# Kernel optimization log

Hardware: AMD Instinct MI355X
Metric: run time of the kernel (lower is better)

## Reference

```python
import jax, jax.numpy as jnp
import numpy as np


def _haar_dwt2(x):
    # x: [b, H, W] -> (ll, lh, hl, hh), each [b, H/2, W/2]; orthonormal 2D Haar
    a = x[:, ::2, ::2]
    b = x[:, ::2, 1::2]
    c = x[:, 1::2, ::2]
    d = x[:, 1::2, 1::2]
    ll = (a + b + c + d) * 0.5
    lh = (a + b - c - d) * 0.5  # detail along rows (frames)
    hl = (a - b + c - d) * 0.5  # detail along cols (features)
    hh = (a - b - c + d) * 0.5
    return ll, lh, hl, hh


def _haar_idwt2(ll, lh, hl, hh):
    a = (ll + lh + hl + hh) * 0.5
    b = (ll + lh - hl - hh) * 0.5
    c = (ll - lh + hl - hh) * 0.5
    d = (ll - lh - hl + hh) * 0.5
    B, H2, W2 = ll.shape
    out = jnp.zeros((B, 2 * H2, 2 * W2), ll.dtype)
    out = out.at[:, ::2, ::2].set(a)
    out = out.at[:, ::2, 1::2].set(b)
    out = out.at[:, 1::2, ::2].set(c)
    out = out.at[:, 1::2, 1::2].set(d)
    return out


def _interp_linear_last(x, m):
    # linear interpolation along last dim from linspace(0,1,n) to linspace(0,1,m)
    n = x.shape[-1]
    pos = jnp.linspace(0.0, 1.0, m, dtype=x.dtype) * (n - 1)
    i0 = jnp.clip(jnp.floor(pos).astype(jnp.int32), 0, n - 2)
    w = pos - i0.astype(x.dtype)
    return x[..., i0] * (1.0 - w) + x[..., i0 + 1] * w


def setup_inputs() -> dict:
    key = jax.random.key(0)
    k0, k1, k2 = jax.random.split(key, 3)
    b, f, c, hidden = 128, 256, 512, 2048
    x = jax.random.normal(k0, (b, f, c), dtype=jnp.float32)
    fc1_w = jax.random.normal(k1, (hidden, c), dtype=jnp.float32) * 0.02
    fc1_b = jnp.zeros((hidden,), dtype=jnp.float32)
    fc2_w = jax.random.normal(k2, (c // 2, hidden), dtype=jnp.float32) * 0.02
    fc2_b = jnp.zeros((c // 2,), dtype=jnp.float32)
    return {"x": x, "fc1_w": fc1_w, "fc1_b": fc1_b, "fc2_w": fc2_w, "fc2_b": fc2_b}


def reference(x, fc1_w, fc1_b, fc2_w, fc2_b):
    b, f, c = x.shape
    ll, lh, hl, hh = _haar_dwt2(x)               # [b, f/2, c/2] each
    ll_up = _interp_linear_last(ll, c)           # [b, f/2, c]
    h = jax.nn.gelu(jnp.einsum('bfc,hc->bfh', ll_up, fc1_w) + fc1_b, approximate=False)
    ll_new = jnp.einsum('bfh,oh->bfo', h, fc2_w) + fc2_b  # [b, f/2, c/2]
    return _haar_idwt2(ll_new, lh, hl, hh)       # [b, f, c]
```

## Files before the change

### kernel.cpp

```cpp
#include <hip/hip_runtime.h>
#include <hip/hip_bf16.h>
#include <stdint.h>

typedef __bf16 bf16;
typedef __attribute__((ext_vector_type(8)))  __bf16 bf16x8;
typedef __attribute__((ext_vector_type(16))) float  f32x16;

#define B_DIM 128
#define F_DIM 256
#define C_DIM 512
#define HID   2048
#define C2    256
#define MROWS 16384

static constexpr size_t OFF_W1 = 0;
static constexpr size_t OFF_W2 = 1u << 20;

__device__ __forceinline__ unsigned short bfbits(float f) {
    bf16 h = (bf16)f;
    return __builtin_bit_cast(unsigned short, h);
}
#define SCHED0() __builtin_amdgcn_sched_barrier(0)

__global__ __launch_bounds__(256) void prep_kernel(
    const float* __restrict__ w1, const float* __restrict__ w2,
    bf16* __restrict__ w1pp, bf16* __restrict__ w2pp)
{
    const int blk = blockIdx.x;
    const int t = threadIdx.x;
    if (blk < 2048) {
        int idx = blk * 256 + t;
        int h = idx >> 8, k = idx & 255;
        const float* wrow = w1 + (size_t)h * C_DIM;
        float acc = 0.f;
        int jlo = (k == 0) ? 0 : (int)((float)(k - 1) * (511.0f / 255.0f));
        int jhi = (int)((float)(k + 1) * (511.0f / 255.0f)) + 1;
        if (jhi > 511) jhi = 511;
        for (int j = jlo; j <= jhi; ++j) {
            float pos = (float)j * (255.0f / 511.0f);
            int i0 = (int)pos;
            if (i0 > 254) i0 = 254;
            float w = pos - (float)i0;
            float coef = (i0 == k) ? (1.0f - w) : ((i0 + 1 == k) ? w : 0.0f);
            acc += coef * wrow[j];
        }
        size_t frag = (size_t)(h >> 5) * 16 + (k >> 4);
        size_t lane = (size_t)(((k >> 3) & 1) << 5 | (h & 31));
        w1pp[frag * 512 + lane * 8 + (k & 7)] = (bf16)acc;
    } else {
        int idx2 = (blk - 2048) * 256 + t;
        int c2 = idx2 >> 11, hid = idx2 & 2047;
        float v = w2[(size_t)c2 * HID + hid];
        size_t frag = (size_t)(c2 >> 5) * 128 + (hid >> 4);
        size_t lane = (size_t)(((hid >> 3) & 1) << 5 | (c2 & 31));
        w2pp[frag * 512 + lane * 8 + (hid & 7)] = (bf16)v;
    }
}

__global__ __launch_bounds__(512, 2) void fused_mlp(
    const bf16* __restrict__ w1pp, const bf16* __restrict__ w2pp,
    const float* __restrict__ b1, const float* __restrict__ b2,
    const float* __restrict__ x, float* __restrict__ out)
{
    __shared__ __align__(16) char smem[49152];
    char* hsm = smem + 16384;

    const int tid = threadIdx.x;
    const int l   = tid & 63;
    const int wv  = tid >> 6;
    const int sub = wv >> 2;
    const int sl4 = wv & 3;
    const int R0  = blockIdx.x * 32;
    const char* w1B = (const char*)w1pp;
    const char* w2B = (const char*)w2pp;

    {
        const int r = tid & 31;
        const int s = tid >> 5;
        const int gbf = R0 + r;
        const float* xr0 = x + ((size_t)(gbf >> 7) * F_DIM + (size_t)(gbf & 127) * 2) * C_DIM;
        const float* xr1 = xr0 + C_DIM;
#pragma unroll
        for (int jj = 0; jj < 2; ++jj) {
            int j = s * 2 + jj;
            float4 a[4], b[4];
#pragma unroll
            for (int i = 0; i < 4; ++i) {
                a[i] = ((const float4*)xr0)[j * 4 + i];
                b[i] = ((const float4*)xr1)[j * 4 + i];
            }
            const float* pa = (const float*)a;
            const float* pb = (const float*)b;
            bf16x8 pk;
#pragma unroll
            for (int e = 0; e < 8; ++e)
                pk[e] = (bf16)(0.5f * (pa[2*e] + pa[2*e+1] + pb[2*e] + pb[2*e+1]));
            *(bf16x8*)(smem + s * 1024 + (size_t)((jj << 5) | r) * 16) = pk;
        }
    }
    __syncthreads();

    bf16x8 llr[16];
#pragma unroll
    for (int kf = 0; kf < 16; ++kf)
        llr[kf] = *(const bf16x8*)(smem + kf * 1024 + (size_t)l * 16);

    f32x16 acc2{};

#pragma unroll 1
    for (int pc = 0; pc < 4; ++pc) {
        f32x16 acc1_0{}, acc1_1{};
        const int hb = pc * 16 + sub * 8 + sl4 * 2;
        const char* w1f = w1B + ((size_t)hb * 16) * 1024 + (size_t)l * 16;
#pragma unroll
        for (int g = 0; g < 2; ++g) {
            bf16x8 wf0[8], wf1[8];
#pragma unroll
            for (int i = 0; i < 8; ++i) {
                wf0[i] = *(const bf16x8*)(w1f + (g * 8 + i) * 1024);
                wf1[i] = *(const bf16x8*)(w1f + (16 + g * 8 + i) * 1024);
            }
            SCHED0();
#pragma unroll
            for (int i = 0; i < 8; ++i) {
                acc1_0 = __builtin_amdgcn_mfma_f32_32x32x16_bf16(llr[g * 8 + i], wf0[i], acc1_0, 0, 0, 0);
                acc1_1 = __builtin_amdgcn_mfma_f32_32x32x16_bf16(llr[g * 8 + i], wf1[i], acc1_1, 0, 0, 0);
            }
        }

#pragma unroll
        for (int nf = 0; nf < 2; ++nf) {
            const f32x16& A = nf ? acc1_1 : acc1_0;
            const int cin = sub * 256 + sl4 * 64 + nf * 32 + (l & 31);
            const float bs = b1[pc * 512 + cin];
            const int kf2 = cin >> 4;
#pragma unroll
            for (int reg = 0; reg < 16; ++reg) {
                float v = A[reg] + bs;
                float tt = v * (0.79788456080f + 0.03567740814f * v * v);
                float g = v / (1.0f + __expf(-2.0f * tt));
                float gp = __builtin_bit_cast(float,
                    __builtin_amdgcn_mov_dpp(__builtin_bit_cast(int, g), 0xB1, 0xF, 0xF, true));
                if (!(l & 1)) {
                    unsigned u = (unsigned)bfbits(g) | ((unsigned)bfbits(gp) << 16);
                    int crow = (reg & 3) + 8 * (reg >> 2) + 4 * (l >> 5);
                    int lane2 = (((l >> 3) & 1) << 5) | crow;
                    *(unsigned*)(hsm + kf2 * 1024 + lane2 * 16 + (l & 7) * 2) = u;
                }
            }
        }
        __syncthreads();

        const char* w2f = w2B + ((size_t)(wv * 128 + pc * 32)) * 1024 + (size_t)l * 16;
#pragma unroll
        for (int g = 0; g < 4; ++g) {
            bf16x8 wf[8];
#pragma unroll
            for (int i = 0; i < 8; ++i)
                wf[i] = *(const bf16x8*)(w2f + (g * 8 + i) * 1024);
            SCHED0();
#pragma unroll
            for (int i = 0; i < 8; ++i) {
                bf16x8 hfr = *(const bf16x8*)(hsm + (g * 8 + i) * 1024 + (size_t)l * 16);
                acc2 = __builtin_amdgcn_mfma_f32_32x32x16_bf16(hfr, wf[i], acc2, 0, 0, 0);
            }
        }
        __syncthreads();
    }

    {
        const int c2 = wv * 32 + (l & 31);
        const float bs = b2[c2];
#pragma unroll
        for (int reg = 0; reg < 16; ++reg) {
            int R = R0 + (reg & 3) + 8 * (reg >> 2) + 4 * (l >> 5);
            int b = R >> 7, f2 = R & 127;
            const float* xr = x + ((size_t)b * F_DIM + (size_t)f2 * 2) * C_DIM;
            float2 p0 = ((const float2*)xr)[c2];
            float2 p1 = ((const float2*)(xr + C_DIM))[c2];
            float llo = 0.5f * (p0.x + p0.y + p1.x + p1.y);
            float d = 0.5f * ((acc2[reg] + bs) - llo);
            float2 o0, o1;
            o0.x = p0.x + d; o0.y = p0.y + d;
            o1.x = p1.x + d; o1.y = p1.y + d;
            float* orow = out + ((size_t)b * F_DIM + (size_t)f2 * 2) * C_DIM;
            ((float2*)orow)[c2] = o0;
            ((float2*)(orow + C_DIM))[c2] = o1;
        }
    }
}

extern "C" void kernel_launch(void* const* d_in, const int* in_sizes, int n_in,
                              void* d_out, int out_size, void* d_ws, size_t ws_size,
                              hipStream_t stream) {
    const float* x     = (const float*)d_in[0];
    const float* fc1_w = (const float*)d_in[1];
    const float* fc1_b = (const float*)d_in[2];
    const float* fc2_w = (const float*)d_in[3];
    const float* fc2_b = (const float*)d_in[4];
    float* out = (float*)d_out;

    char* ws = (char*)d_ws;
    bf16* w1pp = (bf16*)(ws + OFF_W1);
    bf16* w2pp = (bf16*)(ws + OFF_W2);

    prep_kernel<<<4096, 256, 0, stream>>>(fc1_w, fc2_w, w1pp, w2pp);
    fused_mlp<<<MROWS / 32, 512, 0, stream>>>(w1pp, w2pp, fc1_b, fc2_b, x, out);
}
```

Before: 100.8 us.

## Use a 4-deep rolling weight prefetch and raise occupancy in the fused MLP

Replaces the large per-group weight register batches and the 16-register resident activation fragments with a 4-slot rolling prefetch buffer. Each MFMA step issues the weight load for two steps ahead, and the prefetch carries across the fc1/fc2 phase boundary and into the next chunk. Activation fragments are now re-read from shared memory on each step. This cuts register pressure so launch bounds can request 4 blocks per SM instead of 2, trading deep load batching for more resident waves to hide latency. The x loads and the output stores also become nontemporal.

```diff
diff --git a/kernel.cpp b/kernel.cpp
--- a/kernel.cpp
+++ b/kernel.cpp
@@ -5,6 +5,8 @@
 typedef __bf16 bf16;
 typedef __attribute__((ext_vector_type(8)))  __bf16 bf16x8;
 typedef __attribute__((ext_vector_type(16))) float  f32x16;
+typedef __attribute__((ext_vector_type(4)))  float  f32x4v;
+typedef __attribute__((ext_vector_type(2)))  float  f32x2v;
 
 #define B_DIM 128
 #define F_DIM 256
@@ -20,7 +22,6 @@
     bf16 h = (bf16)f;
     return __builtin_bit_cast(unsigned short, h);
 }
-#define SCHED0() __builtin_amdgcn_sched_barrier(0)
 
 __global__ __launch_bounds__(256) void prep_kernel(
     const float* __restrict__ w1, const float* __restrict__ w2,
@@ -57,7 +58,7 @@
     }
 }
 
-__global__ __launch_bounds__(512, 2) void fused_mlp(
+__global__ __launch_bounds__(512, 4) void fused_mlp(
     const bf16* __restrict__ w1pp, const bf16* __restrict__ w2pp,
     const float* __restrict__ b1, const float* __restrict__ b2,
     const float* __restrict__ x, float* __restrict__ out)
@@ -74,6 +75,15 @@
     const char* w1B = (const char*)w1pp;
     const char* w2B = (const char*)w2pp;
 
+    bf16x8 wf[4];
+    {
+        const char* w1f0 = w1B + (size_t)(sub * 8 + sl4 * 2) * 16 * 1024 + (size_t)l * 16;
+        wf[0] = *(const bf16x8*)(w1f0);
+        wf[1] = *(const bf16x8*)(w1f0 + 16 * 1024);
+        wf[2] = *(const bf16x8*)(w1f0 + 1024);
+        wf[3] = *(const bf16x8*)(w1f0 + 16 * 1024 + 1024);
+    }
+
     {
         const int r = tid & 31;
         const int s = tid >> 5;
@@ -83,11 +93,11 @@
 #pragma unroll
         for (int jj = 0; jj < 2; ++jj) {
             int j = s * 2 + jj;
-            float4 a[4], b[4];
+            f32x4v a[4], b[4];
 #pragma unroll
             for (int i = 0; i < 4; ++i) {
-                a[i] = ((const float4*)xr0)[j * 4 + i];
-                b[i] = ((const float4*)xr1)[j * 4 + i];
+                a[i] = __builtin_nontemporal_load((const f32x4v*)(xr0 + (j * 4 + i) * 4));
+                b[i] = __builtin_nontemporal_load((const f32x4v*)(xr1 + (j * 4 + i) * 4));
             }
             const float* pa = (const float*)a;
             const float* pb = (const float*)b;
@@ -100,31 +110,28 @@
     }
     __syncthreads();
 
-    bf16x8 llr[16];
-#pragma unroll
-    for (int kf = 0; kf < 16; ++kf)
-        llr[kf] = *(const bf16x8*)(smem + kf * 1024 + (size_t)l * 16);
-
     f32x16 acc2{};
 
 #pragma unroll 1
     for (int pc = 0; pc < 4; ++pc) {
+        const char* w1f = w1B + (size_t)(pc * 16 + sub * 8 + sl4 * 2) * 16 * 1024 + (size_t)l * 16;
+        const char* w2f = w2B + ((size_t)(wv * 128 + pc * 32)) * 1024 + (size_t)l * 16;
+        const int pn = (pc + 1) & 3;
+        const char* w1fn = w1B + (size_t)(pn * 16 + sub * 8 + sl4 * 2) * 16 * 1024 + (size_t)l * 16;
+
         f32x16 acc1_0{}, acc1_1{};
-        const int hb = pc * 16 + sub * 8 + sl4 * 2;
-        const char* w1f = w1B + ((size_t)hb * 16) * 1024 + (size_t)l * 16;
-#pragma unroll
-        for (int g = 0; g < 2; ++g) {
-            bf16x8 wf0[8], wf1[8];
-#pragma unroll
-            for (int i = 0; i < 8; ++i) {
-                wf0[i] = *(const bf16x8*)(w1f + (g * 8 + i) * 1024);
-                wf1[i] = *(const bf16x8*)(w1f + (16 + g * 8 + i) * 1024);
-            }
-            SCHED0();
-#pragma unroll
-            for (int i = 0; i < 8; ++i) {
-                acc1_0 = __builtin_amdgcn_mfma_f32_32x32x16_bf16(llr[g * 8 + i], wf0[i], acc1_0, 0, 0, 0);
-                acc1_1 = __builtin_amdgcn_mfma_f32_32x32x16_bf16(llr[g * 8 + i], wf1[i], acc1_1, 0, 0, 0);
+#pragma unroll
+        for (int ks = 0; ks < 16; ++ks) {
+            bf16x8 af = *(const bf16x8*)(smem + ks * 1024 + (size_t)l * 16);
+            acc1_0 = __builtin_amdgcn_mfma_f32_32x32x16_bf16(af, wf[(2 * ks) & 3], acc1_0, 0, 0, 0);
+            acc1_1 = __builtin_amdgcn_mfma_f32_32x32x16_bf16(af, wf[(2 * ks + 1) & 3], acc1_1, 0, 0, 0);
+            if (ks < 14) {
+                wf[(2 * ks) & 3]     = *(const bf16x8*)(w1f + (ks + 2) * 1024);
+                wf[(2 * ks + 1) & 3] = *(const bf16x8*)(w1f + 16 * 1024 + (ks + 2) * 1024);
+            } else {
+                int v0 = (ks - 14) * 2;
+                wf[(2 * ks) & 3]     = *(const bf16x8*)(w2f + (v0 + 0) * 1024);
+                wf[(2 * ks + 1) & 3] = *(const bf16x8*)(w2f + (v0 + 1) * 1024);
             }
         }
 
@@ -151,18 +158,15 @@
         }
         __syncthreads();
 
-        const char* w2f = w2B + ((size_t)(wv * 128 + pc * 32)) * 1024 + (size_t)l * 16;
-#pragma unroll
-        for (int g = 0; g < 4; ++g) {
-            bf16x8 wf[8];
-#pragma unroll
-            for (int i = 0; i < 8; ++i)
-                wf[i] = *(const bf16x8*)(w2f + (g * 8 + i) * 1024);
-            SCHED0();
-#pragma unroll
-            for (int i = 0; i < 8; ++i) {
-                bf16x8 hfr = *(const bf16x8*)(hsm + (g * 8 + i) * 1024 + (size_t)l * 16);
-                acc2 = __builtin_amdgcn_mfma_f32_32x32x16_bf16(hfr, wf[i], acc2, 0, 0, 0);
+#pragma unroll
+        for (int v = 0; v < 32; ++v) {
+            bf16x8 hf = *(const bf16x8*)(hsm + v * 1024 + (size_t)l * 16);
+            acc2 = __builtin_amdgcn_mfma_f32_32x32x16_bf16(hf, wf[v & 3], acc2, 0, 0, 0);
+            if (v < 28) {
+                wf[v & 3] = *(const bf16x8*)(w2f + (v + 4) * 1024);
+            } else {
+                int u = v - 28;
+                wf[v & 3] = *(const bf16x8*)(w1fn + (u & 1) * 16 * 1024 + (u >> 1) * 1024);
             }
         }
         __syncthreads();
@@ -176,16 +180,16 @@
             int R = R0 + (reg & 3) + 8 * (reg >> 2) + 4 * (l >> 5);
             int b = R >> 7, f2 = R & 127;
             const float* xr = x + ((size_t)b * F_DIM + (size_t)f2 * 2) * C_DIM;
-            float2 p0 = ((const float2*)xr)[c2];
-            float2 p1 = ((const float2*)(xr + C_DIM))[c2];
-            float llo = 0.5f * (p0.x + p0.y + p1.x + p1.y);
+            f32x2v p0 = __builtin_nontemporal_load((const f32x2v*)(xr + c2 * 2));
+            f32x2v p1 = __builtin_nontemporal_load((const f32x2v*)(xr + C_DIM + c2 * 2));
+            float llo = 0.5f * (p0[0] + p0[1] + p1[0] + p1[1]);
             float d = 0.5f * ((acc2[reg] + bs) - llo);
-            float2 o0, o1;
-            o0.x = p0.x + d; o0.y = p0.y + d;
-            o1.x = p1.x + d; o1.y = p1.y + d;
+            f32x2v o0, o1;
+            o0[0] = p0[0] + d; o0[1] = p0[1] + d;
+            o1[0] = p1[0] + d; o1[1] = p1[1] + d;
             float* orow = out + ((size_t)b * F_DIM + (size_t)f2 * 2) * C_DIM;
-            ((float2*)orow)[c2] = o0;
-            ((float2*)(orow + C_DIM))[c2] = o1;
+            __builtin_nontemporal_store(o0, (f32x2v*)(orow + c2 * 2));
+            __builtin_nontemporal_store(o1, (f32x2v*)(orow + C_DIM + c2 * 2));
         }
     }
 }
```

Result: slower. 110.4 us (+9.5%).
